# Optimization experiments

Measured on AMD Instinct MI355X. Metric: run time of the kernel, lower is better.

The kernel has to match this reference:

```python
import jax, jax.numpy as jnp
import numpy as np

N = 100000   # nodes
E = 800000   # edges (avg degree 8)
D = 128      # input_dim == output_dim
H = 4        # num_heads
DH = D // H  # head_dim = 32


def setup_inputs() -> dict:
    key = jax.random.key(0)
    ks = jax.random.split(key, 12)
    s = 1.0 / np.sqrt(D)
    x = jax.random.normal(ks[0], (N, D), jnp.float32)
    row = jnp.sort(jax.random.randint(ks[1], (E,), 0, N))  # destination (query) nodes
    col = jax.random.randint(ks[2], (E,), 0, N)            # source (key/value) nodes
    Wq = jax.random.normal(ks[3], (D, D), jnp.float32) * s
    bq = jax.random.normal(ks[4], (D,), jnp.float32) * 0.01
    Wk = jax.random.normal(ks[5], (D, D), jnp.float32) * s
    bk = jax.random.normal(ks[6], (D,), jnp.float32) * 0.01
    Wv = jax.random.normal(ks[7], (D, D), jnp.float32) * s
    bv = jax.random.normal(ks[8], (D,), jnp.float32) * 0.01
    Wo = jax.random.normal(ks[9], (D, D), jnp.float32) * s
    bo = jax.random.normal(ks[10], (D,), jnp.float32) * 0.01
    return {"x": x, "row": row, "col": col, "Wq": Wq, "bq": bq, "Wk": Wk,
            "bk": bk, "Wv": Wv, "bv": bv, "Wo": Wo, "bo": bo}


def reference(x, row, col, Wq, bq, Wk, bk, Wv, bv, Wo, bo):
    n = x.shape[0]
    # projections; reshape (N, head_dim, num_heads) exactly as the torch code
    # NOTE: source scales q by k.size(-1)**0.5 == sqrt(num_heads) (quirk, kept faithful)
    scale = jnp.asarray(H, x.dtype) ** 0.5
    q = ((x @ Wq.T + bq).reshape(n, DH, H)) / scale
    k = (x @ Wk.T + bk).reshape(n, DH, H)
    v = (x @ Wv.T + bv).reshape(n, DH, H)
    # bsddmm: per-edge, per-head scores s[e,h] = q[row[e],:,h] . k[col[e],:,h]
    s = jnp.einsum('edh,edh->eh', q[row], k[col])  # (E, H)
    # sparse row-wise softmax over incoming edges of each destination node
    m = jax.ops.segment_max(s, row, num_segments=n)      # (N, H)
    e = jnp.exp(s - m[row])                               # (E, H)
    z = jax.ops.segment_sum(e, row, num_segments=n)      # (N, H)
    a = e / z[row]                                        # (E, H) attention weights
    # bspmm: y[i,:,h] = sum_{e: row[e]=i} a[e,h] * v[col[e],:,h]
    y = jax.ops.segment_sum(a[:, None, :] * v[col], row, num_segments=n)  # (N, DH, H)
    return y.reshape(n, D) @ Wo.T + bo
```

## Files before the change

### kernel.cpp

```cpp
#include <hip/hip_runtime.h>
#include <hip/hip_bf16.h>
#include <hip/hip_fp16.h>
#include <math.h>

#define D 128
#define H 4

typedef __attribute__((ext_vector_type(8))) short bf16x8;
typedef __attribute__((ext_vector_type(4))) float f32x4;

__device__ __forceinline__ unsigned short f32_to_bf16_rne(float f) {
    union { float f; unsigned u; } c; c.f = f;
    unsigned u = c.u;
    return (unsigned short)((u + 0x7FFFu + ((u >> 16) & 1u)) >> 16);
}
__device__ __forceinline__ float bf16_to_f32(unsigned short h) {
    union { unsigned u; float f; } c; c.u = ((unsigned)h) << 16;
    return c.f;
}

__global__ __launch_bounds__(256) void convert_split(
    const float* __restrict__ in, unsigned short* __restrict__ hi,
    unsigned short* __restrict__ lo, int n4)
{
    int i = blockIdx.x * blockDim.x + threadIdx.x;
    if (i >= n4) return;
    float4 v = ((const float4*)in)[i];
    ushort4 h, l;
    h.x = f32_to_bf16_rne(v.x); l.x = f32_to_bf16_rne(v.x - bf16_to_f32(h.x));
    h.y = f32_to_bf16_rne(v.y); l.y = f32_to_bf16_rne(v.y - bf16_to_f32(h.y));
    h.z = f32_to_bf16_rne(v.z); l.z = f32_to_bf16_rne(v.z - bf16_to_f32(h.z));
    h.w = f32_to_bf16_rne(v.w); l.w = f32_to_bf16_rne(v.w - bf16_to_f32(h.w));
    ((ushort4*)hi)[i] = h;
    ((ushort4*)lo)[i] = l;
}

__global__ __launch_bounds__(256) void convert_w(
    const float* __restrict__ Wq, const float* __restrict__ Wk,
    const float* __restrict__ Wv, const float* __restrict__ Wo,
    unsigned short* __restrict__ wh, unsigned short* __restrict__ wl)
{
    int i = blockIdx.x * blockDim.x + threadIdx.x;
    if (i >= D * D) return;
    int r = i >> 7;
    int c = i & 127;
    int pr = ((r & 3) << 5) | (r >> 2);
    int pc = ((c & 3) << 5) | (c >> 2);
    const float* Ws[4] = {Wq, Wk, Wv, Wo};
#pragma unroll
    for (int m = 0; m < 4; ++m) {
        float f = Ws[m][i];
        unsigned short h = f32_to_bf16_rne(f);
        unsigned short l = f32_to_bf16_rne(f - bf16_to_f32(h));
        int dst = (m < 3) ? (pr * D + c) : (r * D + pc);
        wh[m * D * D + dst] = h;
        wl[m * D * D + dst] = l;
    }
}

#define RT 64

__global__ __launch_bounds__(512) void gemm_tile(
    const unsigned short* __restrict__ xh, const unsigned short* __restrict__ xl,
    const unsigned short* __restrict__ whAll, const unsigned short* __restrict__ wlAll,
    const float* __restrict__ b0, const float* __restrict__ b1,
    const float* __restrict__ b2,
    void* __restrict__ o0, void* __restrict__ o1, void* __restrict__ o2,
    float scale0, int n, int wbase, int halfmask, int permBias)
{
    __shared__ unsigned short Ah[RT * 128];
    __shared__ unsigned short Al[RT * 128];

    const int sel = blockIdx.y;
    const unsigned short* wh = whAll + (size_t)(wbase + sel) * D * D;
    const unsigned short* wl = wlAll + (size_t)(wbase + sel) * D * D;
    const float* bias = (sel == 0) ? b0 : (sel == 1 ? b1 : b2);
    void* out        = (sel == 0) ? o0 : (sel == 1 ? o1 : o2);
    const float scale = (sel == 0) ? scale0 : 1.0f;
    const bool halfOut = (halfmask >> sel) & 1;

    const int wid  = threadIdx.x >> 6;
    const int lane = threadIdx.x & 63;
    const int quad = lane >> 4;
    const int l16  = lane & 15;
    const int m0   = blockIdx.x * RT;

    const unsigned short* wrh = wh + (size_t)(wid * 16 + l16) * D + quad * 8;
    const unsigned short* wrl = wl + (size_t)(wid * 16 + l16) * D + quad * 8;
    bf16x8 bh[4], bl[4];
#pragma unroll
    for (int kc = 0; kc < 4; ++kc) {
        bh[kc] = *(const bf16x8*)(wrh + kc * 32);
        bl[kc] = *(const bf16x8*)(wrl + kc * 32);
    }

    for (int idx = threadIdx.x; idx < RT * 16; idx += 512) {
        int r  = idx >> 4;
        int c8 = idx & 15;
        int rg = m0 + r; if (rg > n - 1) rg = n - 1;
        int cs = ((c8 ^ (r & 15)) * 8);
        *(bf16x8*)&Ah[r * 128 + cs] = *(const bf16x8*)(xh + (size_t)rg * D + c8 * 8);
        *(bf16x8*)&Al[r * 128 + cs] = *(const bf16x8*)(xl + (size_t)rg * D + c8 * 8);
    }
    __syncthreads();

    f32x4 acc[4];
#pragma unroll
    for (int rt = 0; rt < 4; ++rt) acc[rt] = (f32x4){0.f, 0.f, 0.f, 0.f};

#pragma unroll
    for (int kc = 0; kc < 4; ++kc) {
        const int cs = ((quad + 4 * kc) ^ l16) * 8;
        bf16x8 ah[4], al[4];
#pragma unroll
        for (int rt = 0; rt < 4; ++rt) {
            const int r = rt * 16 + l16;
            ah[rt] = *(const bf16x8*)&Ah[r * 128 + cs];
            al[rt] = *(const bf16x8*)&Al[r * 128 + cs];
        }
#pragma unroll
        for (int rt = 0; rt < 4; ++rt)
            acc[rt] = __builtin_amdgcn_mfma_f32_16x16x32_bf16(ah[rt], bh[kc], acc[rt], 0, 0, 0);
#pragma unroll
        for (int rt = 0; rt < 4; ++rt)
            acc[rt] = __builtin_amdgcn_mfma_f32_16x16x32_bf16(al[rt], bh[kc], acc[rt], 0, 0, 0);
#pragma unroll
        for (int rt = 0; rt < 4; ++rt)
            acc[rt] = __builtin_amdgcn_mfma_f32_16x16x32_bf16(ah[rt], bl[kc], acc[rt], 0, 0, 0);
    }

    const int colg = wid * 16 + l16;
    const int bidx = permBias ? (((colg & 31) << 2) | (colg >> 5)) : colg;
    const float bv = bias[bidx];
    if (halfOut) {
        __half* oph = (__half*)out;
#pragma unroll
        for (int rt = 0; rt < 4; ++rt) {
#pragma unroll
            for (int r = 0; r < 4; ++r) {
                int rowg = m0 + rt * 16 + quad * 4 + r;
                if (rowg < n)
                    oph[(size_t)rowg * D + colg] = __float2half(acc[rt][r] + bv);
            }
        }
    } else {
        float* opf = (float*)out;
#pragma unroll
        for (int rt = 0; rt < 4; ++rt) {
#pragma unroll
            for (int r = 0; r < 4; ++r) {
                int rowg = m0 + rt * 16 + quad * 4 + r;
                if (rowg < n)
                    opf[(size_t)rowg * D + colg] = (acc[rt][r] + bv) * scale;
            }
        }
    }
}

__global__ void build_row_start(const int* __restrict__ row,
                                int* __restrict__ row_start, int n, int e)
{
    int i = blockIdx.x * blockDim.x + threadIdx.x;
    if (i > n) return;
    int lo = 0, hi = e;
    while (lo < hi) {
        int mid = (lo + hi) >> 1;
        if (row[mid] < i) lo = mid + 1; else hi = mid;
    }
    row_start[i] = lo;
}

#define MAXDEG 64
#define WPB 4

__global__ __launch_bounds__(WPB * 64) void edge_attn(
    const int* __restrict__ row_start,
    const float* __restrict__ q, const __half* __restrict__ k,
    const __half* __restrict__ v, const int* __restrict__ col,
    unsigned short* __restrict__ yh, unsigned short* __restrict__ yl, int n)
{
    __shared__ float ssm[WPB][MAXDEG * H];
    __shared__ int   cm[WPB][MAXDEG];

    const int wid  = threadIdx.x >> 6;
    const int lane = threadIdx.x & 63;
    const int node = blockIdx.x * WPB + wid;
    if (node >= n) return;

    const int e0  = row_start[node];
    const int deg = row_start[node + 1] - e0;

    float acc0 = 0.f, acc1 = 0.f;

    if (deg > MAXDEG) {
        const float q0 = q[(size_t)node * D + 2 * lane];
        const float q1 = q[(size_t)node * D + 2 * lane + 1];
        float m = -INFINITY, z = 0.f;
        for (int e = 0; e < deg; ++e) {
            int c = col[e0 + e];
            __half2 kk = ((const __half2*)(k + ((size_t)c << 7)))[lane];
            float p = q0 * __half2float(kk.x) + q1 * __half2float(kk.y);
            p += __shfl_xor(p, 1);
            p += __shfl_xor(p, 2);
            p += __shfl_xor(p, 4);
            p += __shfl_xor(p, 8);
            float mn = fmaxf(m, p);
            z = z * __expf(m - mn) + __expf(p - mn);
            m = mn;
        }
        const float rz = 1.f / z;
        for (int e = 0; e < deg; ++e) {
            int c = col[e0 + e];
            __half2 kk = ((const __half2*)(k + ((size_t)c << 7)))[lane];
            float p = q0 * __half2float(kk.x) + q1 * __half2float(kk.y);
            p += __shfl_xor(p, 1);
            p += __shfl_xor(p, 2);
            p += __shfl_xor(p, 4);
            p += __shfl_xor(p, 8);
            float a = __expf(p - m) * rz;
            __half2 vv = ((const __half2*)(v + ((size_t)c << 7)))[lane];
            acc0 += a * __half2float(vv.x);
            acc1 += a * __half2float(vv.y);
        }
    } else {
        const int sub = lane & 15;
        const int qe  = lane >> 4;

        for (int i = lane; i < deg; i += 64) cm[wid][i] = col[e0 + i];

        const float4* q4 = (const float4*)(q + (size_t)node * D) + sub * 2;
        const float4 qa = q4[0], qb = q4[1];

        for (int e = 0; e < deg; e += 4) {
            int ei = e + qe;
            int ec = ei < deg ? ei : deg - 1;
            int c  = cm[wid][ec];
            union { bf16x8 v8; __half h[8]; } ku;
            ku.v8 = *(const bf16x8*)(k + ((size_t)c << 7) + sub * 8);
            float p = qa.x * __half2float(ku.h[0]) + qa.y * __half2float(ku.h[1])
                    + qa.z * __half2float(ku.h[2]) + qa.w * __half2float(ku.h[3])
                    + qb.x * __half2float(ku.h[4]) + qb.y * __half2float(ku.h[5])
                    + qb.z * __half2float(ku.h[6]) + qb.w * __half2float(ku.h[7]);
            p += __shfl_xor(p, 1);
            p += __shfl_xor(p, 2);
            if ((sub & 3) == 0 && ei < deg)
                ssm[wid][ei * 4 + (sub >> 2)] = p;
        }

        const int dl4 = deg * 4;
        float vloc[4];
        float mx = -INFINITY;
#pragma unroll
        for (int j = 0; j < 4; ++j) {
            int f = lane + 64 * j;
            vloc[j] = (f < dl4) ? ssm[wid][f] : -INFINITY;
            mx = fmaxf(mx, vloc[j]);
        }
        mx = fmaxf(mx, __shfl_xor(mx, 4));
        mx = fmaxf(mx, __shfl_xor(mx, 8));
        mx = fmaxf(mx, __shfl_xor(mx, 16));
        mx = fmaxf(mx, __shfl_xor(mx, 32));
        float ex[4];
        float zs = 0.f;
#pragma unroll
        for (int j = 0; j < 4; ++j) {
            ex[j] = __expf(vloc[j] - mx);
            if (lane + 64 * j < dl4) zs += ex[j];
        }
        zs += __shfl_xor(zs, 4);
        zs += __shfl_xor(zs, 8);
        zs += __shfl_xor(zs, 16);
        zs += __shfl_xor(zs, 32);
        const float rz = 1.f / zs;
#pragma unroll
        for (int j = 0; j < 4; ++j) {
            int f = lane + 64 * j;
            if (f < dl4) ssm[wid][f] = ex[j] * rz;
        }

        const int hh = lane >> 4;
        int e = 0;
        for (; e + 4 <= deg; e += 4) {
            int c0 = cm[wid][e],     c1 = cm[wid][e + 1];
            int c2 = cm[wid][e + 2], c3 = cm[wid][e + 3];
            float a0 = ssm[wid][e * 4 + hh],       a1 = ssm[wid][(e + 1) * 4 + hh];
            float a2 = ssm[wid][(e + 2) * 4 + hh], a3 = ssm[wid][(e + 3) * 4 + hh];
            __half2 v0 = ((const __half2*)(v + ((size_t)c0 << 7)))[lane];
            __half2 v1 = ((const __half2*)(v + ((size_t)c1 << 7)))[lane];
            __half2 v2 = ((const __half2*)(v + ((size_t)c2 << 7)))[lane];
            __half2 v3 = ((const __half2*)(v + ((size_t)c3 << 7)))[lane];
            acc0 += a0 * __half2float(v0.x) + a1 * __half2float(v1.x)
                  + a2 * __half2float(v2.x) + a3 * __half2float(v3.x);
            acc1 += a0 * __half2float(v0.y) + a1 * __half2float(v1.y)
                  + a2 * __half2float(v2.y) + a3 * __half2float(v3.y);
        }
        for (; e < deg; ++e) {
            int c = cm[wid][e];
            float a = ssm[wid][e * 4 + hh];
            __half2 vv = ((const __half2*)(v + ((size_t)c << 7)))[lane];
            acc0 += a * __half2float(vv.x);
            acc1 += a * __half2float(vv.y);
        }
    }

    unsigned short h0 = f32_to_bf16_rne(acc0);
    unsigned short h1 = f32_to_bf16_rne(acc1);
    ushort2 hi2, lo2;
    hi2.x = h0; hi2.y = h1;
    lo2.x = f32_to_bf16_rne(acc0 - bf16_to_f32(h0));
    lo2.y = f32_to_bf16_rne(acc1 - bf16_to_f32(h1));
    ((ushort2*)yh)[(size_t)node * 64 + lane] = hi2;
    ((ushort2*)yl)[(size_t)node * 64 + lane] = lo2;
}

extern "C" void kernel_launch(void* const* d_in, const int* in_sizes, int n_in,
                              void* d_out, int out_size, void* d_ws, size_t ws_size,
                              hipStream_t stream)
{
    const float* x   = (const float*)d_in[0];
    const int*   row = (const int*)  d_in[1];
    const int*   col = (const int*)  d_in[2];
    const float* Wq  = (const float*)d_in[3];
    const float* bq  = (const float*)d_in[4];
    const float* Wk  = (const float*)d_in[5];
    const float* bk  = (const float*)d_in[6];
    const float* Wv  = (const float*)d_in[7];
    const float* bv  = (const float*)d_in[8];
    const float* Wo  = (const float*)d_in[9];
    const float* bo  = (const float*)d_in[10];
    float* out = (float*)d_out;

    const int n = in_sizes[0] / D;
    const int e = in_sizes[1];
    const size_t ND = (size_t)n * D;

    float* ws = (float*)d_ws;
    float*  q  = ws;
    __half* kh = (__half*)(ws + ND);
    __half* vh = kh + ND;
    unsigned short* xh = (unsigned short*)(ws + 2 * ND);
    unsigned short* xl = xh + ND;
    unsigned short* yh = xh;
    unsigned short* yl = xl;
    unsigned short* wh = (unsigned short*)(ws + 3 * ND);
    unsigned short* wl = wh + 4 * D * D;
    int* row_start = (int*)(wl + 4 * D * D);

    const int n4 = (int)(ND / 4);
    const int gx = (n + RT - 1) / RT;

    convert_w<<<(D * D + 255) / 256, 256, 0, stream>>>(Wq, Wk, Wv, Wo, wh, wl);
    convert_split<<<(n4 + 255) / 256, 256, 0, stream>>>(x, xh, xl, n4);

    gemm_tile<<<dim3(gx, 3), 512, 0, stream>>>(
        xh, xl, wh, wl, bq, bk, bv,
        (void*)q, (void*)kh, (void*)vh, 0.5f, n, 0, 6, 1);

    build_row_start<<<(n + 1 + 255) / 256, 256, 0, stream>>>(row, row_start, n, e);

    edge_attn<<<(n + WPB - 1) / WPB, WPB * 64, 0, stream>>>(
        row_start, q, kh, vh, col, yh, yl, n);

    gemm_tile<<<dim3(gx, 1), 512, 0, stream>>>(
        yh, yl, wh, wl, bo, bo, bo,
        (void*)out, (void*)out, (void*)out, 1.0f, n, 3, 0, 0);
}
```

Baseline: 300.1 us.

## Fuse score, softmax and aggregation into single pass without max subtraction

Merges the per-edge score computation, softmax and V aggregation into one loop per group of four edges. Unnormalised exp weights are broadcast via shuffles and accumulated, then divided by the sum at the end. This removes the shared-memory score buffer, the separate max/sum reductions and the second edge pass, and unifies the high-degree path. Dropping the max subtraction risks exp overflow if scores get large.

```diff
diff --git a/kernel.cpp b/kernel.cpp
--- a/kernel.cpp
+++ b/kernel.cpp
@@ -173,14 +173,64 @@
 #define MAXDEG 64
 #define WPB 4
 
+template<bool BIG>
+__device__ __forceinline__ void edge_loop(
+    int lane, int sub, int grp, int deg, int e0,
+    const int* cmrow, const int* __restrict__ col,
+    const float4 qa, const float4 qb,
+    const __half* __restrict__ k, const __half* __restrict__ v,
+    float& acc0, float& acc1, float& z)
+{
+    for (int e = 0; e < deg; e += 4) {
+        const int ei = e + grp;
+        int c0, c1, c2, c3, cs;
+        if (!BIG) {
+            const int4 cc = *(const int4*)&cmrow[e];
+            c0 = cc.x; c1 = cc.y; c2 = cc.z; c3 = cc.w;
+            cs = cmrow[ei < deg ? ei : deg - 1];
+        } else {
+            int es = ei < deg ? ei : deg - 1;
+            cs = col[e0 + es];
+            int e1 = e + 1 < deg ? e + 1 : deg - 1;
+            int e2 = e + 2 < deg ? e + 2 : deg - 1;
+            int e3 = e + 3 < deg ? e + 3 : deg - 1;
+            c0 = col[e0 + e];
+            c1 = col[e0 + e1];
+            c2 = col[e0 + e2];
+            c3 = col[e0 + e3];
+        }
+        __half2 v0 = ((const __half2*)(v + ((size_t)c0 << 7)))[lane];
+        __half2 v1 = ((const __half2*)(v + ((size_t)c1 << 7)))[lane];
+        __half2 v2 = ((const __half2*)(v + ((size_t)c2 << 7)))[lane];
+        __half2 v3 = ((const __half2*)(v + ((size_t)c3 << 7)))[lane];
+        union { bf16x8 v8; __half hx[8]; } ku;
+        ku.v8 = *(const bf16x8*)(k + ((size_t)cs << 7) + sub * 8);
+        float p = qa.x * __half2float(ku.hx[0]) + qa.y * __half2float(ku.hx[1])
+                + qa.z * __half2float(ku.hx[2]) + qa.w * __half2float(ku.hx[3])
+                + qb.x * __half2float(ku.hx[4]) + qb.y * __half2float(ku.hx[5])
+                + qb.z * __half2float(ku.hx[6]) + qb.w * __half2float(ku.hx[7]);
+        p += __shfl_xor(p, 1);
+        p += __shfl_xor(p, 2);
+        float ep = (ei < deg) ? __expf(p) : 0.f;
+        float a0 = __shfl(ep,      4 * grp);
+        float a1 = __shfl(ep, 16 + 4 * grp);
+        float a2 = __shfl(ep, 32 + 4 * grp);
+        float a3 = __shfl(ep, 48 + 4 * grp);
+        z += (a0 + a1) + (a2 + a3);
+        acc0 += a0 * __half2float(v0.x) + a1 * __half2float(v1.x)
+              + a2 * __half2float(v2.x) + a3 * __half2float(v3.x);
+        acc1 += a0 * __half2float(v0.y) + a1 * __half2float(v1.y)
+              + a2 * __half2float(v2.y) + a3 * __half2float(v3.y);
+    }
+}
+
 __global__ __launch_bounds__(WPB * 64) void edge_attn(
     const int* __restrict__ row_start,
     const float* __restrict__ q, const __half* __restrict__ k,
     const __half* __restrict__ v, const int* __restrict__ col,
     unsigned short* __restrict__ yh, unsigned short* __restrict__ yl, int n)
 {
-    __shared__ float ssm[WPB][MAXDEG * H];
-    __shared__ int   cm[WPB][MAXDEG];
+    __shared__ int cm[WPB][MAXDEG];
 
     const int wid  = threadIdx.x >> 6;
     const int lane = threadIdx.x & 63;
@@ -189,119 +239,30 @@
 
     const int e0  = row_start[node];
     const int deg = row_start[node + 1] - e0;
-
-    float acc0 = 0.f, acc1 = 0.f;
-
-    if (deg > MAXDEG) {
-        const float q0 = q[(size_t)node * D + 2 * lane];
-        const float q1 = q[(size_t)node * D + 2 * lane + 1];
-        float m = -INFINITY, z = 0.f;
-        for (int e = 0; e < deg; ++e) {
-            int c = col[e0 + e];
-            __half2 kk = ((const __half2*)(k + ((size_t)c << 7)))[lane];
-            float p = q0 * __half2float(kk.x) + q1 * __half2float(kk.y);
-            p += __shfl_xor(p, 1);
-            p += __shfl_xor(p, 2);
-            p += __shfl_xor(p, 4);
-            p += __shfl_xor(p, 8);
-            float mn = fmaxf(m, p);
-            z = z * __expf(m - mn) + __expf(p - mn);
-            m = mn;
-        }
-        const float rz = 1.f / z;
-        for (int e = 0; e < deg; ++e) {
-            int c = col[e0 + e];
-            __half2 kk = ((const __half2*)(k + ((size_t)c << 7)))[lane];
-            float p = q0 * __half2float(kk.x) + q1 * __half2float(kk.y);
-            p += __shfl_xor(p, 1);
-            p += __shfl_xor(p, 2);
-            p += __shfl_xor(p, 4);
-            p += __shfl_xor(p, 8);
-            float a = __expf(p - m) * rz;
-            __half2 vv = ((const __half2*)(v + ((size_t)c << 7)))[lane];
-            acc0 += a * __half2float(vv.x);
-            acc1 += a * __half2float(vv.y);
-        }
+    const int sub = lane & 15;
+    const int grp = lane >> 4;
+
+    const float4* q4 = (const float4*)(q + (size_t)node * D) + sub * 2;
+    const float4 qa = q4[0], qb = q4[1];
+
+    float acc0 = 0.f, acc1 = 0.f, z = 0.f;
+
+    if (deg <= MAXDEG) {
+        const int dl4 = (deg + 3) & ~3;
+        for (int i = lane; i < dl4; i += 64) {
+            int ii = i < deg ? i : deg - 1;
+            cm[wid][i] = col[e0 + ii];
+        }
+        edge_loop<false>(lane, sub, grp, deg, e0, cm[wid], col, qa, qb, k, v,
+                         acc0, acc1, z);
     } else {
-        const int sub = lane & 15;
-        const int qe  = lane >> 4;
-
-        for (int i = lane; i < deg; i += 64) cm[wid][i] = col[e0 + i];
-
-        const float4* q4 = (const float4*)(q + (size_t)node * D) + sub * 2;
-        const float4 qa = q4[0], qb = q4[1];
-
-        for (int e = 0; e < deg; e += 4) {
-            int ei = e + qe;
-            int ec = ei < deg ? ei : deg - 1;
-            int c  = cm[wid][ec];
-            union { bf16x8 v8; __half h[8]; } ku;
-            ku.v8 = *(const bf16x8*)(k + ((size_t)c << 7) + sub * 8);
-            float p = qa.x * __half2float(ku.h[0]) + qa.y * __half2float(ku.h[1])
-                    + qa.z * __half2float(ku.h[2]) + qa.w * __half2float(ku.h[3])
-                    + qb.x * __half2float(ku.h[4]) + qb.y * __half2float(ku.h[5])
-                    + qb.z * __half2float(ku.h[6]) + qb.w * __half2float(ku.h[7]);
-            p += __shfl_xor(p, 1);
-            p += __shfl_xor(p, 2);
-            if ((sub & 3) == 0 && ei < deg)
-                ssm[wid][ei * 4 + (sub >> 2)] = p;
-        }
-
-        const int dl4 = deg * 4;
-        float vloc[4];
-        float mx = -INFINITY;
-#pragma unroll
-        for (int j = 0; j < 4; ++j) {
-            int f = lane + 64 * j;
-            vloc[j] = (f < dl4) ? ssm[wid][f] : -INFINITY;
-            mx = fmaxf(mx, vloc[j]);
-        }
-        mx = fmaxf(mx, __shfl_xor(mx, 4));
-        mx = fmaxf(mx, __shfl_xor(mx, 8));
-        mx = fmaxf(mx, __shfl_xor(mx, 16));
-        mx = fmaxf(mx, __shfl_xor(mx, 32));
-        float ex[4];
-        float zs = 0.f;
-#pragma unroll
-        for (int j = 0; j < 4; ++j) {
-            ex[j] = __expf(vloc[j] - mx);
-            if (lane + 64 * j < dl4) zs += ex[j];
-        }
-        zs += __shfl_xor(zs, 4);
-        zs += __shfl_xor(zs, 8);
-        zs += __shfl_xor(zs, 16);
-        zs += __shfl_xor(zs, 32);
-        const float rz = 1.f / zs;
-#pragma unroll
-        for (int j = 0; j < 4; ++j) {
-            int f = lane + 64 * j;
-            if (f < dl4) ssm[wid][f] = ex[j] * rz;
-        }
-
-        const int hh = lane >> 4;
-        int e = 0;
-        for (; e + 4 <= deg; e += 4) {
-            int c0 = cm[wid][e],     c1 = cm[wid][e + 1];
-            int c2 = cm[wid][e + 2], c3 = cm[wid][e + 3];
-            float a0 = ssm[wid][e * 4 + hh],       a1 = ssm[wid][(e + 1) * 4 + hh];
-            float a2 = ssm[wid][(e + 2) * 4 + hh], a3 = ssm[wid][(e + 3) * 4 + hh];
-            __half2 v0 = ((const __half2*)(v + ((size_t)c0 << 7)))[lane];
-            __half2 v1 = ((const __half2*)(v + ((size_t)c1 << 7)))[lane];
-            __half2 v2 = ((const __half2*)(v + ((size_t)c2 << 7)))[lane];
-            __half2 v3 = ((const __half2*)(v + ((size_t)c3 << 7)))[lane];
-            acc0 += a0 * __half2float(v0.x) + a1 * __half2float(v1.x)
-                  + a2 * __half2float(v2.x) + a3 * __half2float(v3.x);
-            acc1 += a0 * __half2float(v0.y) + a1 * __half2float(v1.y)
-                  + a2 * __half2float(v2.y) + a3 * __half2float(v3.y);
-        }
-        for (; e < deg; ++e) {
-            int c = cm[wid][e];
-            float a = ssm[wid][e * 4 + hh];
-            __half2 vv = ((const __half2*)(v + ((size_t)c << 7)))[lane];
-            acc0 += a * __half2float(vv.x);
-            acc1 += a * __half2float(vv.y);
-        }
-    }
+        edge_loop<true>(lane, sub, grp, deg, e0, cm[wid], col, qa, qb, k, v,
+                        acc0, acc1, z);
+    }
+
+    const float rz = (z > 0.f) ? 1.f / z : 0.f;
+    acc0 *= rz;
+    acc1 *= rz;
 
     unsigned short h0 = f32_to_bf16_rne(acc0);
     unsigned short h1 = f32_to_bf16_rne(acc1);
```

New measurement: 293.2 us. 2.3% less time.
